# Kernel optimization log

Hardware: AMD Instinct MI355X
Metric: run time of the kernel (lower is better)

The kernel has to match this reference:

```python
import jax, jax.numpy as jnp
import numpy as np

EMBEDDING_DIM = 64  # matches init_kwargs; temperature = sqrt(embedding_dim)


def setup_inputs() -> dict:
    key = jax.random.key(0)
    k1, k2, k3, k4 = jax.random.split(key, 4)
    B, S, D = 8, 2048, EMBEDDING_DIM
    return {
        "key": jax.random.normal(k1, (B, S, D), dtype=jnp.float32),
        "query": jax.random.normal(k2, (B, S, D), dtype=jnp.float32),
        "value": jax.random.normal(k3, (B, S, D), dtype=jnp.float32),
        "query_attention_mask": jax.random.randint(k4, (B, S), 0, 2, dtype=jnp.int32),
    }


def reference(key, query, value, query_attention_mask):
    # scores: [B, S, S]
    temperature = jnp.sqrt(jnp.asarray(EMBEDDING_DIM, dtype=query.dtype))
    scores = jnp.einsum("bqd,bkd->bqk", query, key) / temperature
    # masked_fill_ fills -inf WHERE mask is True (as in the torch source).
    # mask [B, S] -> broadcast over the query axis to [B, 1, S] -> [B, S, S].
    mask = query_attention_mask.astype(bool)[:, None, :]
    scores = jnp.where(mask, -jnp.inf, scores)
    attention_filter = jax.nn.softmax(scores, axis=-1)
    # dropout p=0.0 (deterministic reference) -> identity
    context = jnp.einsum("bqk,bkd->bqd", attention_filter, value)
    return (context, attention_filter)
```

## Files before the change

### kernel.cpp

```cpp
#include <hip/hip_runtime.h>
#include <hip/hip_bf16.h>
#include <math.h>


typedef short bf16x8 __attribute__((ext_vector_type(8)));
typedef short bf16x4 __attribute__((ext_vector_type(4)));
typedef float f32x4 __attribute__((ext_vector_type(4)));

#define BATCH 8
#define SDIM 2048
#define DDIM 64
#define KBLK 64
#define NBLK (SDIM / KBLK)
#define KSPLIT 4
#define BPW (NBLK / KSPLIT)
#define NROWS (BATCH * SDIM)
#define SCALE 0.125f
#define KSTR 72

__device__ __forceinline__ short f2bf(float f) {
    unsigned x = __float_as_uint(f);
    x = (x + 0x7fffu + ((x >> 16) & 1u)) >> 16;
    return (short)x;
}
__device__ __forceinline__ float fidx(const float4& v, int i) {
    return ((const float*)&v)[i];
}

__global__ __launch_bounds__(256, 4)
void attn_prep(const float* __restrict__ Kg, const float* __restrict__ Vg,
               short* __restrict__ Kbf, short* __restrict__ VTbf,
               float* __restrict__ Ctx)
{
    __shared__ short VTlds[DDIM][KSTR];

    const int wg = blockIdx.x;
    const int b = wg & 7;
    const int kbase = (wg >> 3) * KBLK;
    const int tid = threadIdx.x;

    const float* Kb = Kg + (size_t)b * SDIM * DDIM;
    const float* Vb = Vg + (size_t)b * SDIM * DDIM;

    {
        const int key = tid >> 2, doff = (tid & 3) * 16;
        const float* src = Kb + (size_t)(kbase + key) * DDIM + doff;
        float4 f0 = *(const float4*)(src);
        float4 f1 = *(const float4*)(src + 4);
        float4 f2 = *(const float4*)(src + 8);
        float4 f3 = *(const float4*)(src + 12);
        bf16x8 p0, p1;
        p0[0]=f2bf(f0.x); p0[1]=f2bf(f0.y); p0[2]=f2bf(f0.z); p0[3]=f2bf(f0.w);
        p0[4]=f2bf(f1.x); p0[5]=f2bf(f1.y); p0[6]=f2bf(f1.z); p0[7]=f2bf(f1.w);
        p1[0]=f2bf(f2.x); p1[1]=f2bf(f2.y); p1[2]=f2bf(f2.z); p1[3]=f2bf(f2.w);
        p1[4]=f2bf(f3.x); p1[5]=f2bf(f3.y); p1[6]=f2bf(f3.z); p1[7]=f2bf(f3.w);
        short* dst = Kbf + ((size_t)b * SDIM + kbase + key) * DDIM + doff;
        *(bf16x8*)dst = p0;
        *(bf16x8*)(dst + 8) = p1;
    }

    {
        const int sv_d0 = (tid & 15) * 4, sv_k0 = (tid >> 4) * 4;
        float4 vreg[4];
        #pragma unroll
        for (int i = 0; i < 4; ++i)
            vreg[i] = *(const float4*)(Vb + (size_t)(kbase + sv_k0 + i) * DDIM + sv_d0);
        #pragma unroll
        for (int dd = 0; dd < 4; ++dd) {
            bf16x4 pv;
            pv[0] = f2bf(fidx(vreg[0], dd));
            pv[1] = f2bf(fidx(vreg[1], dd));
            pv[2] = f2bf(fidx(vreg[2], dd));
            pv[3] = f2bf(fidx(vreg[3], dd));
            *(bf16x4*)&VTlds[sv_d0 + dd][sv_k0] = pv;
        }
    }
    __syncthreads();
    {
        const int d = tid >> 2, koff = (tid & 3) * 16;
        bf16x8 a = *(const bf16x8*)&VTlds[d][koff];
        bf16x8 c = *(const bf16x8*)&VTlds[d][koff + 8];
        short* dst = VTbf + ((size_t)b * DDIM + d) * SDIM + kbase + koff;
        *(bf16x8*)dst = a;
        *(bf16x8*)(dst + 8) = c;
    }

    {
        float4* dst = (float4*)Ctx + (size_t)wg * 1024;
        for (int i = tid; i < 1024; i += 256) dst[i] = make_float4(0.f, 0.f, 0.f, 0.f);
    }
}

__global__ __launch_bounds__(256, 4)
void attn_stats(const short* __restrict__ Kbf, const float* __restrict__ Qg,
                const int* __restrict__ Mg, float* __restrict__ part)
{
    __shared__ short Klds[KBLK][KSTR];
    __shared__ int   Mlds[KBLK];

    const int wg = blockIdx.x;
    const int b = wg & 7;
    const int qt = (wg >> 3) & 31;
    const int sp = wg >> 8;
    const int tid = threadIdx.x;
    const int w = tid >> 6, lane = tid & 63, col = lane & 15, quad = lane >> 4;

    const float* Qb = Qg + (size_t)b * SDIM * DDIM;
    const int*   Mb = Mg + (size_t)b * SDIM;

    bf16x8 aq[2];
    {
        const float* qsrc = Qb + (size_t)(qt * 64 + w * 16 + col) * DDIM + quad * 8;
        #pragma unroll
        for (int c = 0; c < 2; ++c) {
            float4 f0 = *(const float4*)(qsrc + c * 32);
            float4 f1 = *(const float4*)(qsrc + c * 32 + 4);
            bf16x8 a;
            a[0]=f2bf(f0.x); a[1]=f2bf(f0.y); a[2]=f2bf(f0.z); a[3]=f2bf(f0.w);
            a[4]=f2bf(f1.x); a[5]=f2bf(f1.y); a[6]=f2bf(f1.z); a[7]=f2bf(f1.w);
            aq[c] = a;
        }
    }

    const int skey = tid >> 2;
    const int sdoff = (tid & 3) * 16;
    const int kb0 = sp * BPW * KBLK;
    const short* Ksp = Kbf + ((size_t)b * SDIM + kb0) * DDIM;

    float lsum[4];
    #pragma unroll
    for (int r = 0; r < 4; ++r) lsum[r] = 0.0f;

    bf16x8 ks0, ks1;
    int mreg = 0;
    {
        const short* src = Ksp + (size_t)skey * DDIM + sdoff;
        ks0 = *(const bf16x8*)src;
        ks1 = *(const bf16x8*)(src + 8);
        if (tid < KBLK) mreg = Mb[kb0 + tid];
    }

    for (int kb = 0; kb < BPW; ++kb) {
        __syncthreads();
        *(bf16x8*)&Klds[skey][sdoff]     = ks0;
        *(bf16x8*)&Klds[skey][sdoff + 8] = ks1;
        if (tid < KBLK) Mlds[tid] = mreg;
        __syncthreads();
        if (kb + 1 < BPW) {
            const short* src = Ksp + (size_t)((kb + 1) * KBLK + skey) * DDIM + sdoff;
            ks0 = *(const bf16x8*)src;
            ks1 = *(const bf16x8*)(src + 8);
            if (tid < KBLK) mreg = Mb[kb0 + (kb + 1) * KBLK + tid];
        }

        #pragma unroll
        for (int t = 0; t < 4; ++t) {
            f32x4 acc = {0.f, 0.f, 0.f, 0.f};
            #pragma unroll
            for (int c = 0; c < 2; ++c) {
                bf16x8 bk = *(const bf16x8*)&Klds[t * 16 + col][c * 32 + quad * 8];
                acc = __builtin_amdgcn_mfma_f32_16x16x32_bf16(aq[c], bk, acc, 0, 0, 0);
            }
            const int mk = Mlds[t * 16 + col];
            #pragma unroll
            for (int r = 0; r < 4; ++r)
                lsum[r] += mk ? 0.0f : __expf(acc[r] * SCALE);
        }
    }

    #pragma unroll
    for (int r = 0; r < 4; ++r) {
        float s = lsum[r];
        s += __shfl_xor(s, 1);
        s += __shfl_xor(s, 2);
        s += __shfl_xor(s, 4);
        s += __shfl_xor(s, 8);
        lsum[r] = s;
    }
    if (col == 0) {
        #pragma unroll
        for (int r = 0; r < 4; ++r)
            part[(size_t)sp * NROWS + b * SDIM + qt * 64 + w * 16 + quad * 4 + r] = lsum[r];
    }
}

__global__ __launch_bounds__(256)
void attn_merge(const float* __restrict__ part, float* __restrict__ stats)
{
    const int t = blockIdx.x * 256 + threadIdx.x;
    if (t < NROWS) {
        float l = part[t] + part[NROWS + t] + part[2 * NROWS + t] + part[3 * NROWS + t];
        stats[t] = 1.0f / l;
    }
}

__global__ __launch_bounds__(256, 4)
void attn_emit(const short* __restrict__ Kbf, const short* __restrict__ VTbf,
               const float* __restrict__ Qg, const int* __restrict__ Mg,
               const float* __restrict__ stats, float* __restrict__ Ctx,
               float* __restrict__ Filt)
{
    __shared__ short Klds[KBLK][KSTR];
    __shared__ short VTlds[DDIM][KSTR];
    __shared__ short Plds[4][16][KSTR];
    __shared__ int   Mlds[KBLK];

    const int wg = blockIdx.x;
    const int b = wg & 7;
    const int qt = (wg >> 3) & 31;
    const int sp = wg >> 8;
    const int tid = threadIdx.x;
    const int w = tid >> 6, lane = tid & 63, col = lane & 15, quad = lane >> 4;

    const float* Qb = Qg + (size_t)b * SDIM * DDIM;
    const int*   Mb = Mg + (size_t)b * SDIM;
    float* Ctxb  = Ctx  + (size_t)b * SDIM * DDIM;
    float* Filtb = Filt + (size_t)b * SDIM * SDIM;

    bf16x8 aq[2];
    {
        const float* qsrc = Qb + (size_t)(qt * 64 + w * 16 + col) * DDIM + quad * 8;
        #pragma unroll
        for (int c = 0; c < 2; ++c) {
            float4 f0 = *(const float4*)(qsrc + c * 32);
            float4 f1 = *(const float4*)(qsrc + c * 32 + 4);
            bf16x8 a;
            a[0]=f2bf(f0.x); a[1]=f2bf(f0.y); a[2]=f2bf(f0.z); a[3]=f2bf(f0.w);
            a[4]=f2bf(f1.x); a[5]=f2bf(f1.y); a[6]=f2bf(f1.z); a[7]=f2bf(f1.w);
            aq[c] = a;
        }
    }

    float invl[4];
    #pragma unroll
    for (int r = 0; r < 4; ++r)
        invl[r] = stats[b * SDIM + qt * 64 + w * 16 + quad * 4 + r];

    const int skey = tid >> 2;
    const int sdoff = (tid & 3) * 16;
    const int kb0 = sp * BPW * KBLK;
    const short* Ksp = Kbf + ((size_t)b * SDIM + kb0) * DDIM;
    const short* VTb = VTbf + (size_t)b * DDIM * SDIM;
    const int vd = tid >> 2, vkoff = (tid & 3) * 16;

    f32x4 Oacc[4];
    #pragma unroll
    for (int dt = 0; dt < 4; ++dt) Oacc[dt] = (f32x4){0.f, 0.f, 0.f, 0.f};

    bf16x8 ks0, ks1, vt0, vt1;
    int mreg = 0;
    {
        const short* srck = Ksp + (size_t)skey * DDIM + sdoff;
        ks0 = *(const bf16x8*)srck;
        ks1 = *(const bf16x8*)(srck + 8);
        const short* srcv = VTb + (size_t)vd * SDIM + kb0 + vkoff;
        vt0 = *(const bf16x8*)srcv;
        vt1 = *(const bf16x8*)(srcv + 8);
        if (tid < KBLK) mreg = Mb[kb0 + tid];
    }

    for (int kb = 0; kb < BPW; ++kb) {
        const int kbase = kb0 + kb * KBLK;
        __syncthreads();
        *(bf16x8*)&Klds[skey][sdoff]      = ks0;
        *(bf16x8*)&Klds[skey][sdoff + 8]  = ks1;
        *(bf16x8*)&VTlds[vd][vkoff]       = vt0;
        *(bf16x8*)&VTlds[vd][vkoff + 8]   = vt1;
        if (tid < KBLK) Mlds[tid] = mreg;
        __syncthreads();
        if (kb + 1 < BPW) {
            const short* srck = Ksp + (size_t)((kb + 1) * KBLK + skey) * DDIM + sdoff;
            ks0 = *(const bf16x8*)srck;
            ks1 = *(const bf16x8*)(srck + 8);
            const short* srcv = VTb + (size_t)vd * SDIM + (kbase + KBLK) + vkoff;
            vt0 = *(const bf16x8*)srcv;
            vt1 = *(const bf16x8*)(srcv + 8);
            if (tid < KBLK) mreg = Mb[kbase + KBLK + tid];
        }

        #pragma unroll
        for (int t = 0; t < 4; ++t) {
            f32x4 acc = {0.f, 0.f, 0.f, 0.f};
            #pragma unroll
            for (int c = 0; c < 2; ++c) {
                bf16x8 bk = *(const bf16x8*)&Klds[t * 16 + col][c * 32 + quad * 8];
                acc = __builtin_amdgcn_mfma_f32_16x16x32_bf16(aq[c], bk, acc, 0, 0, 0);
            }
            const int mk = Mlds[t * 16 + col];
            #pragma unroll
            for (int r = 0; r < 4; ++r) {
                float p = mk ? 0.0f : __expf(acc[r] * SCALE) * invl[r];
                __builtin_nontemporal_store(
                    p, &Filtb[(size_t)(qt * 64 + w * 16 + quad * 4 + r) * SDIM + kbase + t * 16 + col]);
                Plds[w][quad * 4 + r][t * 16 + col] = f2bf(p);
            }
        }

        #pragma unroll
        for (int c = 0; c < 2; ++c) {
            bf16x8 ap = *(const bf16x8*)&Plds[w][col][c * 32 + quad * 8];
            #pragma unroll
            for (int dt = 0; dt < 4; ++dt) {
                bf16x8 bv = *(const bf16x8*)&VTlds[dt * 16 + col][c * 32 + quad * 8];
                Oacc[dt] = __builtin_amdgcn_mfma_f32_16x16x32_bf16(ap, bv, Oacc[dt], 0, 0, 0);
            }
        }
    }

    #pragma unroll
    for (int dt = 0; dt < 4; ++dt) {
        #pragma unroll
        for (int r = 0; r < 4; ++r) {
            unsafeAtomicAdd(&Ctxb[(size_t)(qt * 64 + w * 16 + quad * 4 + r) * DDIM + dt * 16 + col],
                            Oacc[dt][r]);
        }
    }
}

extern "C" void kernel_launch(void* const* d_in, const int* in_sizes, int n_in,
                              void* d_out, int out_size, void* d_ws, size_t ws_size,
                              hipStream_t stream) {
    const float* Kg = (const float*)d_in[0];
    const float* Qg = (const float*)d_in[1];
    const float* Vg = (const float*)d_in[2];
    const int*   Mg = (const int*)d_in[3];
    float* Ctx  = (float*)d_out;
    float* Filt = (float*)d_out + (size_t)BATCH * SDIM * DDIM;

    short* Kbf  = (short*)d_ws;
    short* VTbf = Kbf + (size_t)BATCH * SDIM * DDIM;
    float* part  = (float*)(VTbf + (size_t)BATCH * DDIM * SDIM);
    float* stats = part + (size_t)KSPLIT * NROWS;

    attn_prep<<<dim3(BATCH * NBLK), dim3(256), 0, stream>>>(Kg, Vg, Kbf, VTbf, Ctx);
    attn_stats<<<dim3(BATCH * NBLK * KSPLIT), dim3(256), 0, stream>>>(Kbf, Qg, Mg, part);
    attn_merge<<<dim3(NROWS / 256), dim3(256), 0, stream>>>(part, stats);
    attn_emit<<<dim3(BATCH * NBLK * KSPLIT), dim3(256), 0, stream>>>(Kbf, VTbf, Qg, Mg, stats, Ctx, Filt);
}
```

Measured before the change: 187.9 us.

## Drop LDS staging of K/V/mask and double the key split

The stats and emit kernels stop staging K, V^T and the mask through shared memory behind block-wide barriers. Each lane now loads its MFMA operands directly from global memory and relies on the L1/L2 caches for reuse. The key dimension split rises from 4 to 8 to give more workgroups, and the launch-bound occupancy hints are raised to match. This removes barrier and LDS traffic, but adds redundant, less coalesced global loads and more partial-sum and atomic work in the merge and context accumulation.

Measured after the change: 258.1 us. 37.3% more time.

```diff
diff --git a/kernel.cpp b/kernel.cpp
--- a/kernel.cpp
+++ b/kernel.cpp
@@ -12,7 +12,7 @@
 #define DDIM 64
 #define KBLK 64
 #define NBLK (SDIM / KBLK)
-#define KSPLIT 4
+#define KSPLIT 8
 #define BPW (NBLK / KSPLIT)
 #define NROWS (BATCH * SDIM)
 #define SCALE 0.125f
@@ -91,13 +91,10 @@
     }
 }
 
-__global__ __launch_bounds__(256, 4)
+__global__ __launch_bounds__(256, 8)
 void attn_stats(const short* __restrict__ Kbf, const float* __restrict__ Qg,
                 const int* __restrict__ Mg, float* __restrict__ part)
 {
-    __shared__ short Klds[KBLK][KSTR];
-    __shared__ int   Mlds[KBLK];
-
     const int wg = blockIdx.x;
     const int b = wg & 7;
     const int qt = (wg >> 3) & 31;
@@ -107,6 +104,7 @@
 
     const float* Qb = Qg + (size_t)b * SDIM * DDIM;
     const int*   Mb = Mg + (size_t)b * SDIM;
+    const short* Kb = Kbf + (size_t)b * SDIM * DDIM;
 
     bf16x8 aq[2];
     {
@@ -122,46 +120,23 @@
         }
     }
 
-    const int skey = tid >> 2;
-    const int sdoff = (tid & 3) * 16;
     const int kb0 = sp * BPW * KBLK;
-    const short* Ksp = Kbf + ((size_t)b * SDIM + kb0) * DDIM;
-
     float lsum[4];
     #pragma unroll
     for (int r = 0; r < 4; ++r) lsum[r] = 0.0f;
 
-    bf16x8 ks0, ks1;
-    int mreg = 0;
-    {
-        const short* src = Ksp + (size_t)skey * DDIM + sdoff;
-        ks0 = *(const bf16x8*)src;
-        ks1 = *(const bf16x8*)(src + 8);
-        if (tid < KBLK) mreg = Mb[kb0 + tid];
-    }
-
     for (int kb = 0; kb < BPW; ++kb) {
-        __syncthreads();
-        *(bf16x8*)&Klds[skey][sdoff]     = ks0;
-        *(bf16x8*)&Klds[skey][sdoff + 8] = ks1;
-        if (tid < KBLK) Mlds[tid] = mreg;
-        __syncthreads();
-        if (kb + 1 < BPW) {
-            const short* src = Ksp + (size_t)((kb + 1) * KBLK + skey) * DDIM + sdoff;
-            ks0 = *(const bf16x8*)src;
-            ks1 = *(const bf16x8*)(src + 8);
-            if (tid < KBLK) mreg = Mb[kb0 + (kb + 1) * KBLK + tid];
-        }
-
+        const int kbase = kb0 + kb * KBLK;
         #pragma unroll
         for (int t = 0; t < 4; ++t) {
+            const short* krow = Kb + (size_t)(kbase + t * 16 + col) * DDIM + quad * 8;
             f32x4 acc = {0.f, 0.f, 0.f, 0.f};
             #pragma unroll
             for (int c = 0; c < 2; ++c) {
-                bf16x8 bk = *(const bf16x8*)&Klds[t * 16 + col][c * 32 + quad * 8];
+                bf16x8 bk = *(const bf16x8*)(krow + c * 32);
                 acc = __builtin_amdgcn_mfma_f32_16x16x32_bf16(aq[c], bk, acc, 0, 0, 0);
             }
-            const int mk = Mlds[t * 16 + col];
+            const int mk = Mb[kbase + t * 16 + col];
             #pragma unroll
             for (int r = 0; r < 4; ++r)
                 lsum[r] += mk ? 0.0f : __expf(acc[r] * SCALE);
@@ -189,21 +164,20 @@
 {
     const int t = blockIdx.x * 256 + threadIdx.x;
     if (t < NROWS) {
-        float l = part[t] + part[NROWS + t] + part[2 * NROWS + t] + part[3 * NROWS + t];
+        float l = 0.f;
+        #pragma unroll
+        for (int sp = 0; sp < KSPLIT; ++sp) l += part[(size_t)sp * NROWS + t];
         stats[t] = 1.0f / l;
     }
 }
 
-__global__ __launch_bounds__(256, 4)
+__global__ __launch_bounds__(256, 6)
 void attn_emit(const short* __restrict__ Kbf, const short* __restrict__ VTbf,
                const float* __restrict__ Qg, const int* __restrict__ Mg,
                const float* __restrict__ stats, float* __restrict__ Ctx,
                float* __restrict__ Filt)
 {
-    __shared__ short Klds[KBLK][KSTR];
-    __shared__ short VTlds[DDIM][KSTR];
     __shared__ short Plds[4][16][KSTR];
-    __shared__ int   Mlds[KBLK];
 
     const int wg = blockIdx.x;
     const int b = wg & 7;
@@ -214,6 +188,8 @@
 
     const float* Qb = Qg + (size_t)b * SDIM * DDIM;
     const int*   Mb = Mg + (size_t)b * SDIM;
+    const short* Kb = Kbf + (size_t)b * SDIM * DDIM;
+    const short* VTb = VTbf + (size_t)b * DDIM * SDIM;
     float* Ctxb  = Ctx  + (size_t)b * SDIM * DDIM;
     float* Filtb = Filt + (size_t)b * SDIM * SDIM;
 
@@ -236,57 +212,24 @@
     for (int r = 0; r < 4; ++r)
         invl[r] = stats[b * SDIM + qt * 64 + w * 16 + quad * 4 + r];
 
-    const int skey = tid >> 2;
-    const int sdoff = (tid & 3) * 16;
     const int kb0 = sp * BPW * KBLK;
-    const short* Ksp = Kbf + ((size_t)b * SDIM + kb0) * DDIM;
-    const short* VTb = VTbf + (size_t)b * DDIM * SDIM;
-    const int vd = tid >> 2, vkoff = (tid & 3) * 16;
-
     f32x4 Oacc[4];
     #pragma unroll
     for (int dt = 0; dt < 4; ++dt) Oacc[dt] = (f32x4){0.f, 0.f, 0.f, 0.f};
-
-    bf16x8 ks0, ks1, vt0, vt1;
-    int mreg = 0;
-    {
-        const short* srck = Ksp + (size_t)skey * DDIM + sdoff;
-        ks0 = *(const bf16x8*)srck;
-        ks1 = *(const bf16x8*)(srck + 8);
-        const short* srcv = VTb + (size_t)vd * SDIM + kb0 + vkoff;
-        vt0 = *(const bf16x8*)srcv;
-        vt1 = *(const bf16x8*)(srcv + 8);
-        if (tid < KBLK) mreg = Mb[kb0 + tid];
-    }
 
     for (int kb = 0; kb < BPW; ++kb) {
         const int kbase = kb0 + kb * KBLK;
-        __syncthreads();
-        *(bf16x8*)&Klds[skey][sdoff]      = ks0;
-        *(bf16x8*)&Klds[skey][sdoff + 8]  = ks1;
-        *(bf16x8*)&VTlds[vd][vkoff]       = vt0;
-        *(bf16x8*)&VTlds[vd][vkoff + 8]   = vt1;
-        if (tid < KBLK) Mlds[tid] = mreg;
-        __syncthreads();
-        if (kb + 1 < BPW) {
-            const short* srck = Ksp + (size_t)((kb + 1) * KBLK + skey) * DDIM + sdoff;
-            ks0 = *(const bf16x8*)srck;
-            ks1 = *(const bf16x8*)(srck + 8);
-            const short* srcv = VTb + (size_t)vd * SDIM + (kbase + KBLK) + vkoff;
-            vt0 = *(const bf16x8*)srcv;
-            vt1 = *(const bf16x8*)(srcv + 8);
-            if (tid < KBLK) mreg = Mb[kbase + KBLK + tid];
-        }
 
         #pragma unroll
         for (int t = 0; t < 4; ++t) {
+            const short* krow = Kb + (size_t)(kbase + t * 16 + col) * DDIM + quad * 8;
             f32x4 acc = {0.f, 0.f, 0.f, 0.f};
             #pragma unroll
             for (int c = 0; c < 2; ++c) {
-                bf16x8 bk = *(const bf16x8*)&Klds[t * 16 + col][c * 32 + quad * 8];
+                bf16x8 bk = *(const bf16x8*)(krow + c * 32);
                 acc = __builtin_amdgcn_mfma_f32_16x16x32_bf16(aq[c], bk, acc, 0, 0, 0);
             }
-            const int mk = Mlds[t * 16 + col];
+            const int mk = Mb[kbase + t * 16 + col];
             #pragma unroll
             for (int r = 0; r < 4; ++r) {
                 float p = mk ? 0.0f : __expf(acc[r] * SCALE) * invl[r];
@@ -301,7 +244,8 @@
             bf16x8 ap = *(const bf16x8*)&Plds[w][col][c * 32 + quad * 8];
             #pragma unroll
             for (int dt = 0; dt < 4; ++dt) {
-                bf16x8 bv = *(const bf16x8*)&VTlds[dt * 16 + col][c * 32 + quad * 8];
+                const short* vrow = VTb + (size_t)(dt * 16 + col) * SDIM + kbase + c * 32 + quad * 8;
+                bf16x8 bv = *(const bf16x8*)vrow;
                 Oacc[dt] = __builtin_amdgcn_mfma_f32_16x16x32_bf16(ap, bv, Oacc[dt], 0, 0, 0);
             }
         }
```
